# Performance work log

Hardware: AMD Instinct MI355X
Metric: run time of the kernel (lower is better)

The kernel has to match this reference:

```python
import jax, jax.numpy as jnp
import numpy as np

B, S, I, H, O = 64, 1024, 512, 1024, 256


def setup_inputs() -> dict:
    key = jax.random.key(0)
    ks = jax.random.split(key, 6)
    scale_x = 1.0 / np.sqrt(I)
    scale_h = 1.0 / np.sqrt(H)
    return {
        "x": jax.random.normal(ks[0], (B, S, I), dtype=jnp.float32),
        "Wx": jax.random.normal(ks[1], (H, I), dtype=jnp.float32) * scale_x,
        "Wh": jax.random.normal(ks[2], (H, H), dtype=jnp.float32) * scale_h,
        "b": jax.random.normal(ks[3], (H,), dtype=jnp.float32) * scale_h,
        "Wout": jax.random.normal(ks[4], (O, H), dtype=jnp.float32) * scale_h,
        "bout": jax.random.normal(ks[5], (O,), dtype=jnp.float32) * scale_h,
    }


def reference(x, Wx, Wh, b, Wout, bout):
    # x: [B, S, I]. The original module is per-sequence (S, I); batch is the
    # vmapped leading axis, expressed here directly as batched GEMMs.
    # Precompute input projections for all timesteps in one big GEMM.
    x_proj = jnp.einsum('bsi,hi->sbh', x, Wx) + b  # [S, B, H]

    def step(h, xp_t):  # h: [B, H], xp_t: [B, H]
        h_new = jnp.tanh(xp_t + h @ Wh.T)
        return h_new, h_new

    h0 = jnp.zeros((x.shape[0], Wh.shape[0]), dtype=x.dtype)
    h_last, all_outs = jax.lax.scan(step, h0, x_proj)  # all_outs: [S, B, H]
    y = h_last @ Wout.T + bout  # linear readout of last hidden state
    return y, all_outs
```

## Files before the change

kernel.cpp:

```cpp
#include <hip/hip_runtime.h>
#include <stdint.h>

#define B_ 64
#define S_ 1024
#define I_ 512
#define H_ 1024
#define O_ 256

typedef float f32x4 __attribute__((ext_vector_type(4)));
typedef short s16x8 __attribute__((ext_vector_type(8)));
typedef _Float16 h16x8 __attribute__((ext_vector_type(8)));
typedef unsigned long long u64;
typedef unsigned int u32;

__device__ __forceinline__ float bf2f(unsigned short u) {
    union { unsigned int i; float f; } c; c.i = ((unsigned int)u) << 16; return c.f;
}
__device__ __forceinline__ unsigned short f2bf(float f) {
    union { float f; unsigned int i; } c; c.f = f;
    unsigned int u = c.i;
    return (unsigned short)((u + 0x7fffu + ((u >> 16) & 1u)) >> 16);
}

__device__ __forceinline__ h16x8 load8_h(const void* p, size_t eidx, int isf32) {
    h16x8 r;
    if (isf32) {
        const float* f = (const float*)p + eidx;
        const f32x4 a = *(const f32x4*)f;
        const f32x4 b = *(const f32x4*)(f + 4);
        r[0] = (_Float16)a[0]; r[1] = (_Float16)a[1]; r[2] = (_Float16)a[2]; r[3] = (_Float16)a[3];
        r[4] = (_Float16)b[0]; r[5] = (_Float16)b[1]; r[6] = (_Float16)b[2]; r[7] = (_Float16)b[3];
    } else {
        const s16x8 v = *(const s16x8*)((const unsigned short*)p + eidx);
#pragma unroll
        for (int e = 0; e < 8; ++e) r[e] = (_Float16)bf2f((unsigned short)v[e]);
    }
    return r;
}
__device__ __forceinline__ float load1_f(const void* p, size_t eidx, int isf32) {
    return isf32 ? ((const float*)p)[eidx] : bf2f(((const unsigned short*)p)[eidx]);
}
__device__ __forceinline__ void store1_o(void* p, size_t eidx, float v, int isf32) {
    if (isf32) ((float*)p)[eidx] = v;
    else       ((unsigned short*)p)[eidx] = f2bf(v);
}

__device__ __forceinline__ u64 al64(const u64* p) {
    return __hip_atomic_load(p, __ATOMIC_RELAXED, __HIP_MEMORY_SCOPE_AGENT);
}
__device__ __forceinline__ u32 al32(const u32* p) {
    return __hip_atomic_load(p, __ATOMIC_RELAXED, __HIP_MEMORY_SCOPE_AGENT);
}
__device__ __forceinline__ void as32(u32* p, u32 v) {
    __hip_atomic_store(p, v, __ATOMIC_RELAXED, __HIP_MEMORY_SCOPE_AGENT);
}
__device__ __forceinline__ u32 f16bits(float f) {
    _Float16 h = (_Float16)f;
    union { _Float16 h; unsigned short u; } c; c.h = h; return (u32)c.u;
}

__global__ void detect_kernel(const unsigned int* __restrict__ x, unsigned int* __restrict__ flag) {
    int lane = threadIdx.x;
    int cnt = 0;
#pragma unroll
    for (int i = 0; i < 4; ++i) {
        unsigned int w = x[lane * 4 + i];
        unsigned int e2 = (w >> 7) & 0xFFu;
        cnt += (e2 >= 110u && e2 <= 135u) ? 1 : 0;
    }
#pragma unroll
    for (int d = 1; d < 64; d <<= 1) cnt += __shfl_xor(cnt, d);
    if (lane == 0) *flag = (cnt < 160) ? 1u : 0u;
}

__global__ void zero_kernel(unsigned int* p, int n) {
    int i = blockIdx.x * blockDim.x + threadIdx.x;
    for (; i < n; i += gridDim.x * blockDim.x) p[i] = 0u;
}

__global__ __launch_bounds__(64) void scan_kernel(
        const void* __restrict__ x, const void* __restrict__ Wx,
        const void* __restrict__ Wh, const void* __restrict__ bias,
        _Float16* __restrict__ hbuf, void* __restrict__ out,
        u32* __restrict__ counters, const u32* __restrict__ flagp)
{
    __shared__ _Float16 whs[16 * 1024];
    __shared__ _Float16 wxs[16 * 512];
    const int tid = threadIdx.x;
    const int g = blockIdx.x >> 6;
    const int j = blockIdx.x & 63;
    const int l15 = tid & 15, quad = tid >> 4;
    const int isf32 = (int)*flagp;

    for (int c = tid; c < 2048; c += 64) {
        int n = c >> 7, kb = c & 127;
        h16x8 v = load8_h(Wh, (size_t)(j * 16 + n) * H_ + kb * 8, isf32);
        *(h16x8*)&whs[n * 1024 + ((kb ^ (n & 7)) * 8)] = v;
    }
    for (int c = tid; c < 1024; c += 64) {
        int n = c >> 6, kb = c & 63;
        h16x8 v = load8_h(Wx, (size_t)(j * 16 + n) * I_ + kb * 8, isf32);
        *(h16x8*)&wxs[n * 512 + ((kb ^ (n & 7)) * 8)] = v;
    }
    const float bv = load1_f(bias, j * 16 + l15, isf32);
    u32* cnt = counters + g * 256;
    const int col = j * 16 + l15;
    __syncthreads();

    for (int t = 0; t < S_; ++t) {
        f32x4 acc0 = (f32x4)0.0f, acc1 = (f32x4)0.0f;
#pragma unroll 4
        for (int ks = 0; ks < 16; ++ks) {
            h16x8 a = load8_h(x, ((size_t)(g * 16 + l15) * S_ + t) * I_ + ks * 32 + quad * 8, isf32);
            int kb = (ks * 4 + quad) ^ (l15 & 7);
            h16x8 w = *(const h16x8*)&wxs[l15 * 512 + kb * 8];
            if (ks & 1) acc1 = __builtin_amdgcn_mfma_f32_16x16x32_f16(a, w, acc1, 0, 0, 0);
            else        acc0 = __builtin_amdgcn_mfma_f32_16x16x32_f16(a, w, acc0, 0, 0, 0);
        }

        if (tid == 0 && t) {
            const u32 tgt = 64u * (u32)t;
            for (;;) {
                u32 s = 0;
#pragma unroll
                for (int k2 = 0; k2 < 8; ++k2) s += al32(cnt + k2 * 32);
                if (s >= tgt) break;
                __builtin_amdgcn_s_sleep(1);
            }
        }
        asm volatile("" ::: "memory");

        const u64* hsrc = (const u64*)(hbuf + (size_t)(t & 1) * B_ * H_ + (size_t)g * 16 * H_);
        const int rbase = l15 * 256 + quad * 2;
        u64 qa[16], qb[16];
#define RLOAD(arr, blk) \
        _Pragma("unroll") \
        for (int f = 0; f < 8; ++f) { \
            int wi = rbase + ((blk) * 8 + f) * 8; \
            arr[2 * f]     = al64(hsrc + wi); \
            arr[2 * f + 1] = al64(hsrc + wi + 1); \
        }
#define RMFMA(arr, blk) \
        _Pragma("unroll") \
        for (int f = 0; f < 8; ++f) { \
            int ks = (blk) * 8 + f; \
            union { u64 q[2]; h16x8 v; } u_; \
            u_.q[0] = arr[2 * f]; u_.q[1] = arr[2 * f + 1]; \
            int kb = (ks * 4 + quad) ^ (l15 & 7); \
            h16x8 w = *(const h16x8*)&whs[l15 * 1024 + kb * 8]; \
            if (f & 1) acc1 = __builtin_amdgcn_mfma_f32_16x16x32_f16(u_.v, w, acc1, 0, 0, 0); \
            else       acc0 = __builtin_amdgcn_mfma_f32_16x16x32_f16(u_.v, w, acc0, 0, 0, 0); \
        }
        RLOAD(qa, 0)
        RLOAD(qb, 1)
        RMFMA(qa, 0)
        RLOAD(qa, 2)
        RMFMA(qb, 1)
        RLOAD(qb, 3)
        RMFMA(qa, 2)
        RMFMA(qb, 3)
#undef RLOAD
#undef RMFMA

        f32x4 acc = acc0 + acc1;
        float hv[4];
#pragma unroll
        for (int r = 0; r < 4; ++r) hv[r] = tanhf(acc[r] + bv);

        u32* hw = (u32*)(hbuf + (size_t)((t + 1) & 1) * B_ * H_);
        const int cw = j * 8 + (l15 >> 1);
#pragma unroll
        for (int r = 0; r < 4; ++r) {
            float ov = __shfl_xor(hv[r], 1);
            u32 lo = f16bits((l15 & 1) ? ov : hv[r]);
            u32 hi = f16bits((l15 & 1) ? hv[r] : ov);
            as32(hw + (size_t)(g * 16 + quad * 4 + r) * 512 + cw, lo | (hi << 16));
        }
        asm volatile("s_waitcnt vmcnt(0)" ::: "memory");
        if (tid == 0)
            __hip_atomic_fetch_add(cnt + (j & 7) * 32, 1u,
                                   __ATOMIC_RELAXED, __HIP_MEMORY_SCOPE_AGENT);

#pragma unroll
        for (int r = 0; r < 4; ++r) {
            int brow = g * 16 + quad * 4 + r;
            store1_o(out, (size_t)B_ * O_ + ((size_t)t * B_ + brow) * H_ + col, hv[r], isf32);
        }
    }
}

__global__ __launch_bounds__(64) void readout_kernel(
        const _Float16* __restrict__ hfin, const void* __restrict__ Wout,
        const void* __restrict__ bout, void* __restrict__ y,
        const u32* __restrict__ flagp)
{
    const int tid = threadIdx.x;
    const int tm = blockIdx.x & 3, tn = blockIdx.x >> 2;
    const int l15 = tid & 15, quad = tid >> 4;
    const int isf32 = (int)*flagp;
    f32x4 acc = (f32x4)0.0f;
#pragma unroll 4
    for (int ks = 0; ks < 32; ++ks) {
        h16x8 a = *(const h16x8*)(hfin + (size_t)(tm * 16 + l15) * H_ + ks * 32 + quad * 8);
        h16x8 w = load8_h(Wout, (size_t)(tn * 16 + l15) * H_ + ks * 32 + quad * 8, isf32);
        acc = __builtin_amdgcn_mfma_f32_16x16x32_f16(a, w, acc, 0, 0, 0);
    }
    const int col = tn * 16 + l15;
    const float bo = load1_f(bout, col, isf32);
#pragma unroll
    for (int r = 0; r < 4; ++r) {
        int row = tm * 16 + quad * 4 + r;
        store1_o(y, (size_t)row * O_ + col, acc[r] + bo, isf32);
    }
}

extern "C" void kernel_launch(void* const* d_in, const int* in_sizes, int n_in,
                              void* d_out, int out_size, void* d_ws, size_t ws_size,
                              hipStream_t stream)
{
    const void* x    = d_in[0];
    const void* Wx   = d_in[1];
    const void* Wh   = d_in[2];
    const void* bias = d_in[3];
    const void* Wout = d_in[4];
    const void* bout = d_in[5];

    const size_t HBUF_BYTES = (size_t)2 * B_ * H_ * 2;
    const size_t CNT_BYTES  = 4096;
    char* w = (char*)d_ws;
    _Float16* hbuf     = (_Float16*)w;
    u32*      counters = (u32*)(w + HBUF_BYTES);
    u32*      flag     = (u32*)(w + HBUF_BYTES + CNT_BYTES);

    zero_kernel<<<128, 256, 0, stream>>>((unsigned int*)w, (int)((HBUF_BYTES + CNT_BYTES) / 4));
    detect_kernel<<<1, 64, 0, stream>>>((const unsigned int*)x, flag);

    scan_kernel<<<256, 64, 0, stream>>>(x, Wx, Wh, bias, hbuf, d_out, counters, flag);
    readout_kernel<<<64, 64, 0, stream>>>(hbuf, Wout, bout, d_out, flag);
}
```

Before: 12.71 ms.

## Replace atomic counters with per-block ready flags and batch h loads

Replaces the shared atomic-add counters with a per-block ready-flag array. All 64 lanes poll the 64 flags and combine the result with a wave-wide vote, which removes atomic contention and the serial poll done by one thread. The hidden-state reads now issue all 32 dwordx4 loads up front with cache-bypass bits, splitting the waits so half the MFMAs can start early. It also uses four accumulators and an exp2-based tanh approximation, which trades some accuracy for fewer instructions.

Measured after the change: 11.99 ms. 1.06x faster.

```diff
diff --git a/kernel.cpp b/kernel.cpp
--- a/kernel.cpp
+++ b/kernel.cpp
@@ -45,9 +45,6 @@
     else       ((unsigned short*)p)[eidx] = f2bf(v);
 }
 
-__device__ __forceinline__ u64 al64(const u64* p) {
-    return __hip_atomic_load(p, __ATOMIC_RELAXED, __HIP_MEMORY_SCOPE_AGENT);
-}
 __device__ __forceinline__ u32 al32(const u32* p) {
     return __hip_atomic_load(p, __ATOMIC_RELAXED, __HIP_MEMORY_SCOPE_AGENT);
 }
@@ -57,6 +54,11 @@
 __device__ __forceinline__ u32 f16bits(float f) {
     _Float16 h = (_Float16)f;
     union { _Float16 h; unsigned short u; } c; c.h = h; return (u32)c.u;
+}
+
+__device__ __forceinline__ float tanh_fast(float x) {
+    float e = __builtin_exp2f(x * 2.885390081777927f);
+    return 1.0f - 2.0f / (e + 1.0f);
 }
 
 __global__ void detect_kernel(const unsigned int* __restrict__ x, unsigned int* __restrict__ flag) {
@@ -82,7 +84,7 @@
         const void* __restrict__ x, const void* __restrict__ Wx,
         const void* __restrict__ Wh, const void* __restrict__ bias,
         _Float16* __restrict__ hbuf, void* __restrict__ out,
-        u32* __restrict__ counters, const u32* __restrict__ flagp)
+        u32* __restrict__ rdy_base, const u32* __restrict__ flagp)
 {
     __shared__ _Float16 whs[16 * 1024];
     __shared__ _Float16 wxs[16 * 512];
@@ -103,83 +105,71 @@
         *(h16x8*)&wxs[n * 512 + ((kb ^ (n & 7)) * 8)] = v;
     }
     const float bv = load1_f(bias, j * 16 + l15, isf32);
-    u32* cnt = counters + g * 256;
+    u32* rdy = rdy_base + g * 64;
     const int col = j * 16 + l15;
     __syncthreads();
 
     for (int t = 0; t < S_; ++t) {
-        f32x4 acc0 = (f32x4)0.0f, acc1 = (f32x4)0.0f;
+        f32x4 acc[4] = {(f32x4)0.0f, (f32x4)0.0f, (f32x4)0.0f, (f32x4)0.0f};
 #pragma unroll 4
         for (int ks = 0; ks < 16; ++ks) {
             h16x8 a = load8_h(x, ((size_t)(g * 16 + l15) * S_ + t) * I_ + ks * 32 + quad * 8, isf32);
             int kb = (ks * 4 + quad) ^ (l15 & 7);
             h16x8 w = *(const h16x8*)&wxs[l15 * 512 + kb * 8];
-            if (ks & 1) acc1 = __builtin_amdgcn_mfma_f32_16x16x32_f16(a, w, acc1, 0, 0, 0);
-            else        acc0 = __builtin_amdgcn_mfma_f32_16x16x32_f16(a, w, acc0, 0, 0, 0);
-        }
-
-        if (tid == 0 && t) {
-            const u32 tgt = 64u * (u32)t;
+            acc[ks & 3] = __builtin_amdgcn_mfma_f32_16x16x32_f16(a, w, acc[ks & 3], 0, 0, 0);
+        }
+
+        if (t) {
+            const u32 tgt = (u32)t;
             for (;;) {
-                u32 s = 0;
-#pragma unroll
-                for (int k2 = 0; k2 < 8; ++k2) s += al32(cnt + k2 * 32);
-                if (s >= tgt) break;
+                u32 f = al32(rdy + tid);
+                if (__all(f >= tgt)) break;
                 __builtin_amdgcn_s_sleep(1);
             }
         }
         asm volatile("" ::: "memory");
 
-        const u64* hsrc = (const u64*)(hbuf + (size_t)(t & 1) * B_ * H_ + (size_t)g * 16 * H_);
-        const int rbase = l15 * 256 + quad * 2;
-        u64 qa[16], qb[16];
-#define RLOAD(arr, blk) \
-        _Pragma("unroll") \
-        for (int f = 0; f < 8; ++f) { \
-            int wi = rbase + ((blk) * 8 + f) * 8; \
-            arr[2 * f]     = al64(hsrc + wi); \
-            arr[2 * f + 1] = al64(hsrc + wi + 1); \
-        }
-#define RMFMA(arr, blk) \
-        _Pragma("unroll") \
-        for (int f = 0; f < 8; ++f) { \
-            int ks = (blk) * 8 + f; \
-            union { u64 q[2]; h16x8 v; } u_; \
-            u_.q[0] = arr[2 * f]; u_.q[1] = arr[2 * f + 1]; \
-            int kb = (ks * 4 + quad) ^ (l15 & 7); \
-            h16x8 w = *(const h16x8*)&whs[l15 * 1024 + kb * 8]; \
-            if (f & 1) acc1 = __builtin_amdgcn_mfma_f32_16x16x32_f16(u_.v, w, acc1, 0, 0, 0); \
-            else       acc0 = __builtin_amdgcn_mfma_f32_16x16x32_f16(u_.v, w, acc0, 0, 0, 0); \
-        }
-        RLOAD(qa, 0)
-        RLOAD(qb, 1)
-        RMFMA(qa, 0)
-        RLOAD(qa, 2)
-        RMFMA(qb, 1)
-        RLOAD(qb, 3)
-        RMFMA(qa, 2)
-        RMFMA(qb, 3)
-#undef RLOAD
-#undef RMFMA
-
-        f32x4 acc = acc0 + acc1;
+        const char* hsrc = (const char*)(hbuf + (size_t)(t & 1) * B_ * H_ + (size_t)g * 16 * H_);
+        const u32 voff = (u32)(l15 * 2048 + quad * 16);
+        h16x8 hst[32];
+#pragma unroll
+        for (int ks = 0; ks < 32; ++ks)
+            asm volatile("global_load_dwordx4 %0, %1, %2 offset:%3 sc0 sc1"
+                         : "=v"(hst[ks]) : "v"(voff), "s"(hsrc), "i"(ks * 64) : "memory");
+
+        asm volatile("s_waitcnt vmcnt(16)" ::: "memory");
+        __builtin_amdgcn_sched_barrier(0);
+#pragma unroll
+        for (int ks = 0; ks < 16; ++ks) {
+            int kb = (ks * 4 + quad) ^ (l15 & 7);
+            h16x8 w = *(const h16x8*)&whs[l15 * 1024 + kb * 8];
+            acc[ks & 3] = __builtin_amdgcn_mfma_f32_16x16x32_f16(hst[ks], w, acc[ks & 3], 0, 0, 0);
+        }
+        asm volatile("s_waitcnt vmcnt(0)" ::: "memory");
+        __builtin_amdgcn_sched_barrier(0);
+#pragma unroll
+        for (int ks = 16; ks < 32; ++ks) {
+            int kb = (ks * 4 + quad) ^ (l15 & 7);
+            h16x8 w = *(const h16x8*)&whs[l15 * 1024 + kb * 8];
+            acc[ks & 3] = __builtin_amdgcn_mfma_f32_16x16x32_f16(hst[ks], w, acc[ks & 3], 0, 0, 0);
+        }
+
+        f32x4 accs = (acc[0] + acc[1]) + (acc[2] + acc[3]);
         float hv[4];
 #pragma unroll
-        for (int r = 0; r < 4; ++r) hv[r] = tanhf(acc[r] + bv);
-
-        u32* hw = (u32*)(hbuf + (size_t)((t + 1) & 1) * B_ * H_);
+        for (int r = 0; r < 4; ++r) hv[r] = tanh_fast(accs[r] + bv);
+
+        u32* hw_ = (u32*)(hbuf + (size_t)((t + 1) & 1) * B_ * H_);
         const int cw = j * 8 + (l15 >> 1);
 #pragma unroll
         for (int r = 0; r < 4; ++r) {
             float ov = __shfl_xor(hv[r], 1);
             u32 lo = f16bits((l15 & 1) ? ov : hv[r]);
             u32 hi = f16bits((l15 & 1) ? hv[r] : ov);
-            as32(hw + (size_t)(g * 16 + quad * 4 + r) * 512 + cw, lo | (hi << 16));
+            as32(hw_ + (size_t)(g * 16 + quad * 4 + r) * 512 + cw, lo | (hi << 16));
         }
         asm volatile("s_waitcnt vmcnt(0)" ::: "memory");
-        if (tid == 0)
-            __hip_atomic_fetch_add(cnt + (j & 7) * 32, 1u,
-                                   __ATOMIC_RELAXED, __HIP_MEMORY_SCOPE_AGENT);
+        if (tid == 0) as32(rdy + j, (u32)(t + 1));
 
 #pragma unroll
         for (int r = 0; r < 4; ++r) {
@@ -228,13 +218,13 @@
     const size_t HBUF_BYTES = (size_t)2 * B_ * H_ * 2;
     const size_t CNT_BYTES  = 4096;
     char* w = (char*)d_ws;
-    _Float16* hbuf     = (_Float16*)w;
-    u32*      counters = (u32*)(w + HBUF_BYTES);
-    u32*      flag     = (u32*)(w + HBUF_BYTES + CNT_BYTES);
+    _Float16* hbuf = (_Float16*)w;
+    u32*      rdy  = (u32*)(w + HBUF_BYTES);
+    u32*      flag = (u32*)(w + HBUF_BYTES + CNT_BYTES);
 
     zero_kernel<<<128, 256, 0, stream>>>((unsigned int*)w, (int)((HBUF_BYTES + CNT_BYTES) / 4));
     detect_kernel<<<1, 64, 0, stream>>>((const unsigned int*)x, flag);
 
-    scan_kernel<<<256, 64, 0, stream>>>(x, Wx, Wh, bias, hbuf, d_out, counters, flag);
+    scan_kernel<<<256, 64, 0, stream>>>(x, Wx, Wh, bias, hbuf, d_out, rdy, flag);
     readout_kernel<<<64, 64, 0, stream>>>(hbuf, Wout, bout, d_out, flag);
 }
```
